# Optimization experiments

Measured on AMD Instinct MI355X. Metric: run time of the kernel, lower is better.

## Reference

```python
import jax, jax.numpy as jnp
import numpy as np

B, S, H = 32, 255, 1024
BS, WD, O = 120, 20, 10
HSZ = 2 * (BS + 1) + WD  # 262


def setup_inputs() -> dict:
    key = jax.random.key(0)
    ks = jax.random.split(key, 9)
    inv = lambda *d: 1.0 / np.sqrt(d[0])
    return {
        "state": jax.random.normal(ks[0], (B, S, H), jnp.float32),
        "head_w": jax.random.normal(ks[1], (H, BS), jnp.float32) * inv(H),
        "head_b": jax.random.normal(ks[2], (BS,), jnp.float32) * 0.02,
        "tail_w": jax.random.normal(ks[3], (H, BS), jnp.float32) * inv(H),
        "tail_b": jax.random.normal(ks[4], (BS,), jnp.float32) * 0.02,
        "U": jax.random.normal(ks[5], (O, BS, BS), jnp.float32) * inv(BS),
        "width_table": jax.random.normal(ks[6], (256, WD), jnp.float32).at[0].set(0.0),  # padding_idx=0
        "cls_w": jax.random.normal(ks[7], (O, HSZ), jnp.float32) * inv(HSZ),
        "cls_b": jax.random.normal(ks[8], (O,), jnp.float32) * 0.02,
    }


def _leaky_relu(x):
    return jnp.where(x >= 0, x, 0.01 * x)  # torch LeakyReLU default slope


def reference(state, head_w, head_b, tail_w, tail_b, U, width_table, cls_w, cls_b):
    b, s, _ = state.shape
    bs = head_w.shape[1]
    # head/tail MLPs (dropout is identity in eval)
    h = _leaky_relu(state @ head_w + head_b)  # (b, s, bs)
    t = _leaky_relu(state @ tail_w + tail_b)  # (b, s, bs)

    # bilinear term
    scores1 = jnp.einsum('bxi,oij,byj->bxyo', h, U, t)  # (b, s, s, O)

    # append bias-ones feature
    ones = jnp.ones((b, s, 1), h.dtype)
    h1 = jnp.concatenate([h, ones], axis=-1)  # (b, s, bs+1)
    t1 = jnp.concatenate([t, ones], axis=-1)

    # span-width embedding: pos[x, y] = y - x + 1, clamped to 0 for y < x
    pos = jnp.arange(s)[None, :] - jnp.arange(s)[:, None] + 1
    pos = pos * (pos > 0)
    wemb = width_table[pos]  # (s, s, WD)

    # cls(concat(h1_x, t1_y, wemb_xy)) decomposed into three small projections
    # + broadcast-add; mathematically identical to materializing affined_cat.
    Wh = cls_w[:, :bs + 1]              # (O, bs+1)
    Wt = cls_w[:, bs + 1:2 * (bs + 1)]  # (O, bs+1)
    Ww = cls_w[:, 2 * (bs + 1):]        # (O, WD)
    scores2 = (jnp.einsum('bxi,oi->bxo', h1, Wh)[:, :, None, :]
               + jnp.einsum('byi,oi->byo', t1, Wt)[:, None, :, :]
               + jnp.einsum('xyw,ow->xyo', wemb, Ww)[None]
               + cls_b)
    return scores1 + scores2
```

## Files before the change

### kernel.cpp

```cpp
#include <hip/hip_runtime.h>
#include <hip/hip_bf16.h>

using f32x4 = __attribute__((ext_vector_type(4))) float;
using s16x8 = __attribute__((ext_vector_type(8))) short;
using s16x4 = __attribute__((ext_vector_type(4))) short;

constexpr int RTOT = 32 * 255;

__device__ inline unsigned short f2bf(float x) {
    __hip_bfloat16 b = __float2bfloat16(x);
    return __builtin_bit_cast(unsigned short, b);
}
__device__ inline float bf2f(unsigned short u) {
    unsigned int t = ((unsigned int)u) << 16;
    return __builtin_bit_cast(float, t);
}
__device__ inline f32x4 mfma16(s16x8 a, s16x8 b, f32x4 c) {
    return __builtin_amdgcn_mfma_f32_16x16x32_bf16(a, b, c, 0, 0, 0);
}
__device__ inline void gload16(const unsigned short* g, unsigned short* l) {
    __builtin_amdgcn_global_load_lds(
        (const __attribute__((address_space(1))) void*)g,
        (__attribute__((address_space(3))) void*)l, 16, 0, 0);
}


__global__ __launch_bounds__(256) void convert_k(
    const float* __restrict__ head_w, const float* __restrict__ tail_w,
    const float* __restrict__ U, const float* __restrict__ wtab,
    const float* __restrict__ cls_w,
    unsigned short* __restrict__ WP, unsigned short* __restrict__ Ut,
    float* __restrict__ tblp)
{
    const int tid = threadIdx.x;
    if (blockIdx.x < 16) {
        __shared__ unsigned short Lw[64][258];
        const int ks = blockIdx.x;
        for (int idx = tid; idx < 64 * 16; idx += 256) {
            int r = idx >> 4, c = idx & 15;
            Lw[r][120 + ((c >= 8) ? 128 : 0) + (c & 7)] = 0;
        }
        for (int idx = tid; idx < 7680; idx += 256) {
            int r = idx / 120, c = idx - r * 120;
            Lw[r][c] = f2bf(head_w[(ks * 64 + r) * 120 + c]);
        }
        for (int idx = tid; idx < 7680; idx += 256) {
            int r = idx / 120, c = idx - r * 120;
            Lw[r][128 + c] = f2bf(tail_w[(ks * 64 + r) * 120 + c]);
        }
        __syncthreads();
        for (int item = tid; item < 2048; item += 256) {
            int n = item >> 3, kcp = item & 7;
            int kc = kcp ^ (n & 7);
            s16x8 v;
            #pragma unroll
            for (int e = 0; e < 8; ++e) v[e] = (short)Lw[kc * 8 + e][n];
            *(s16x8*)&WP[ks * 16384 + item * 8] = v;
        }
    } else {
        int gid = (blockIdx.x - 16) * 256 + tid;
        if (gid < 163840) {
            int j = gid & 127, i2 = (gid >> 7) & 127, o = gid >> 14;
            float v = (i2 < 120 && j < 120) ? U[((size_t)o * 120 + i2) * 120 + j] : 0.f;
            Ut[(size_t)o * 16384 + (size_t)j * 128 + i2] = f2bf(v);
        } else {
            int id = gid - 163840;
            if (id < 2560) {
                int p = id / 10, o = id - (id / 10) * 10;
                float s = 0.f;
                #pragma unroll
                for (int wq = 0; wq < 20; ++wq)
                    s += wtab[p * 20 + wq] * cls_w[o * 262 + 242 + wq];
                tblp[p * 12 + o] = s;
            }
        }
    }
}

__global__ __launch_bounds__(512) void ht_mfma(
    const float* __restrict__ state, const unsigned short* __restrict__ WP,
    const float* __restrict__ head_b, const float* __restrict__ tail_b,
    const float* __restrict__ cls_w, const float* __restrict__ cls_b,
    unsigned short* __restrict__ hbuf, unsigned short* __restrict__ tbuf,
    float* __restrict__ hwp, float* __restrict__ twp)
{
    __shared__ unsigned short Ss[2][32 * 64];
    __shared__ unsigned short Ws[2][256 * 64];
    const int r0 = blockIdx.x * 32;
    const int tid = threadIdx.x;
    const int w = tid >> 6, lane = tid & 63;
    const int l16 = lane & 15, kq = lane >> 4;
    const int srow = (tid >> 3) & 31, skc = tid & 7;
    const bool do_s = tid < 256;
    const float* sp = &state[(size_t)(r0 + srow) * 1024 + skc * 8];

    f32x4 acc[2][2];
    #pragma unroll
    for (int fn = 0; fn < 2; ++fn)
        #pragma unroll
        for (int fr = 0; fr < 2; ++fr) acc[fn][fr] = (f32x4){0.f, 0.f, 0.f, 0.f};

    #pragma unroll
    for (int j = 0; j < 4; ++j) {
        int off = (w * 4 + j) * 512;
        gload16(WP + off + lane * 8, &Ws[0][off]);
    }
    if (do_s) {
        f32x4 a0 = *(const f32x4*)sp;
        f32x4 a1 = *(const f32x4*)(sp + 4);
        s16x8 pk;
        #pragma unroll
        for (int e = 0; e < 4; ++e) { pk[e] = (short)f2bf(a0[e]); pk[e + 4] = (short)f2bf(a1[e]); }
        *(s16x8*)((char*)&Ss[0][0] + srow * 128 + ((skc * 16) ^ ((srow & 7) << 4))) = pk;
    }
    __syncthreads();

    for (int it = 0; it < 16; ++it) {
        const int cur = it & 1;
        f32x4 a0, a1;
        if (it < 15) {
            #pragma unroll
            for (int j = 0; j < 4; ++j) {
                int off = (w * 4 + j) * 512;
                gload16(WP + (it + 1) * 16384 + off + lane * 8, &Ws[cur ^ 1][off]);
            }
            if (do_s) {
                a0 = *(const f32x4*)(sp + (it + 1) * 64);
                a1 = *(const f32x4*)(sp + (it + 1) * 64 + 4);
            }
        }
        const char* SsB = (const char*)&Ss[cur][0];
        const char* WsB = (const char*)&Ws[cur][0];
        s16x8 bf[2][2];
        #pragma unroll
        for (int fr = 0; fr < 2; ++fr) {
            int rr = fr * 16 + l16;
            #pragma unroll
            for (int ks = 0; ks < 2; ++ks)
                bf[fr][ks] = *(const s16x8*)(SsB + rr * 128 + ((ks * 64 + kq * 16) ^ ((rr & 7) << 4)));
        }
        #pragma unroll
        for (int fn = 0; fn < 2; ++fn) {
            int n = w * 32 + fn * 16 + l16;
            #pragma unroll
            for (int ks = 0; ks < 2; ++ks) {
                s16x8 af = *(const s16x8*)(WsB + n * 128 + ((ks * 64 + kq * 16) ^ ((n & 7) << 4)));
                #pragma unroll
                for (int fr = 0; fr < 2; ++fr)
                    acc[fn][fr] = mfma16(af, bf[fr][ks], acc[fn][fr]);
            }
        }
        if (it < 15 && do_s) {
            s16x8 pk;
            #pragma unroll
            for (int e = 0; e < 4; ++e) { pk[e] = (short)f2bf(a0[e]); pk[e + 4] = (short)f2bf(a1[e]); }
            *(s16x8*)((char*)&Ss[cur ^ 1][0] + srow * 128 + ((skc * 16) ^ ((srow & 7) << 4))) = pk;
        }
        __syncthreads();
    }

    unsigned short* Hl = &Ws[0][0];
    unsigned short* Tl = &Ws[1][0];
    #pragma unroll
    for (int fn = 0; fn < 2; ++fn) {
        const int n0 = w * 32 + fn * 16 + kq * 4;
        const int isT = n0 >= 128;
        const int c0 = n0 & 127;
        const int g = c0 >> 3, sub = c0 & 7;
        const float* bp = isT ? tail_b : head_b;
        unsigned short* dstl = isT ? Tl : Hl;
        unsigned short* dstg = isT ? tbuf : hbuf;
        #pragma unroll
        for (int fr = 0; fr < 2; ++fr) {
            const int rloc = fr * 16 + l16;
            const int r = r0 + rloc;
            s16x4 pk;
            #pragma unroll
            for (int e = 0; e < 4; ++e) {
                float bv = (c0 + e < 120) ? bp[c0 + e] : 0.f;
                float z = acc[fn][fr][e] + bv;
                z = (z >= 0.f) ? z : 0.01f * z;
                pk[e] = (short)f2bf(z);
            }
            *(s16x4*)&dstl[rloc * 128 + ((g ^ (rloc & 7)) << 3) + sub] = pk;
            {
                int bq = r / 255, x = r - bq * 255;
                *(s16x4*)&dstg[((size_t)bq * 256 + x) * 128 + ((g ^ (x & 7)) << 3) + sub] = pk;
            }
        }
    }
    __syncthreads();

    float* Wl = (float*)&Ws[0][4096];
    for (int idx = tid; idx < 2430; idx += 512) {
        if (idx < 2420) {
            int which = idx / 1210, rem = idx - which * 1210;
            int o = rem / 121, i = rem - o * 121;
            Wl[idx] = cls_w[o * 262 + which * 121 + i];
        } else Wl[idx] = cls_b[idx - 2420];
    }
    __syncthreads();

    for (int d = tid; d < 640; d += 512) {
        int which = d / 320, rem = d - which * 320;
        int rr = rem / 10, o = rem - rr * 10;
        const unsigned short* row = (which ? Tl : Hl) + rr * 128;
        const float* wp2 = &Wl[which * 1210 + o * 121];
        float s = 0.f;
        #pragma unroll
        for (int c = 0; c < 15; ++c) {
            s16x8 v = *(const s16x8*)&row[(c ^ (rr & 7)) << 3];
            #pragma unroll
            for (int e = 0; e < 8; ++e)
                s += bf2f((unsigned short)v[e]) * wp2[c * 8 + e];
        }
        s += wp2[120];
        int gr = r0 + rr;
        if (!which) hwp[(size_t)gr * 12 + o] = s + Wl[2420 + o];
        else        twp[(size_t)gr * 12 + o] = s;
    }
}

__global__ __launch_bounds__(512) void main_mfma(
    const unsigned short* __restrict__ hbuf, const unsigned short* __restrict__ tbuf,
    const unsigned short* __restrict__ Ut,
    const float* __restrict__ hwp, const float* __restrict__ twp,
    const float* __restrict__ tblp, float* __restrict__ out)
{
    __shared__ __align__(16) char smem[124416];
    unsigned short* hUs = (unsigned short*)smem;
    unsigned short* Bs  = (unsigned short*)smem;
    unsigned short* Hs  = (unsigned short*)(smem + 65536);
    float* Ts = (float*)(smem + 98304);
    float* Tb = (float*)(smem + 110592);
    float* Hw = (float*)(smem + 122880);

    const int wgid = blockIdx.x + (blockIdx.y << 3);
    const int virt = (wgid & 7) * 32 + (wgid >> 3);
    const int b = virt >> 3, mg = virt & 7;
    const int tid = threadIdx.x;
    const int w = tid >> 6, lane = tid & 63;
    const int l16 = lane & 15, kq = lane >> 4;
    const int wm = w >> 2, wy = w & 3;
    const size_t tbase = (size_t)b * 256 * 128;
    const size_t hbase = ((size_t)b * 256 + mg * 32) * 128;

    #pragma unroll
    for (int j = 0; j < 8; ++j) {
        int off = (w * 8 + j) * 512;
        gload16(&tbuf[tbase + off + lane * 8], &Bs[off]);
    }
    gload16(&hbuf[hbase + (size_t)(w * 64 + lane) * 8], &Hs[w * 512]);
    {
        const float* twb = twp + (size_t)b * 3060;
        for (int idx = tid; idx < 3060; idx += 512) Ts[idx] = twb[idx];
        for (int idx = tid; idx < 3072; idx += 512) Tb[idx] = tblp[idx];
        if (tid < 384) {
            int mgl = mg * 384 + tid;
            Hw[tid] = (mgl < 3060) ? hwp[(size_t)b * 3060 + mgl] : 0.f;
        }
    }
    __syncthreads();

    s16x8 bfr[4][4];
    #pragma unroll
    for (int ks = 0; ks < 4; ++ks)
        #pragma unroll
        for (int fy = 0; fy < 4; ++fy) {
            int row = wy * 64 + fy * 16 + l16;
            bfr[ks][fy] = *(const s16x8*)((const char*)Bs + row * 256 +
                           ((ks * 64 + kq * 16) ^ ((row & 7) << 4)));
        }
    s16x8 bh[2][4];
    #pragma unroll
    for (int xf = 0; xf < 2; ++xf) {
        int rr = xf * 16 + l16;
        #pragma unroll
        for (int ks = 0; ks < 4; ++ks)
            bh[xf][ks] = *(const s16x8*)((const char*)Hs + rr * 256 +
                          ((ks * 64 + kq * 16) ^ ((rr & 7) << 4)));
    }
    __syncthreads();

    {
        const int jrow = w * 16 + l16;
        const int j0 = w * 16 + kq * 4;
        const int g2 = j0 >> 3, sub2b = (j0 & 7) * 2;
        #pragma unroll 2
        for (int o = 0; o < 10; ++o) {
            f32x4 acc1[2];
            acc1[0] = (f32x4){0.f, 0.f, 0.f, 0.f};
            acc1[1] = (f32x4){0.f, 0.f, 0.f, 0.f};
            #pragma unroll
            for (int ks = 0; ks < 4; ++ks) {
                s16x8 af = *(const s16x8*)&Ut[(size_t)o * 16384 +
                            (size_t)jrow * 128 + ks * 32 + kq * 8];
                acc1[0] = mfma16(af, bh[0][ks], acc1[0]);
                acc1[1] = mfma16(af, bh[1][ks], acc1[1]);
            }
            #pragma unroll
            for (int xf = 0; xf < 2; ++xf) {
                int mloc = (xf * 16 + l16) * 12 + o;
                s16x4 pk;
                #pragma unroll
                for (int e = 0; e < 4; ++e) pk[e] = (short)f2bf(acc1[xf][e]);
                *(s16x4*)((char*)hUs + mloc * 256 +
                          ((g2 ^ (mloc & 7)) << 4) + sub2b) = pk;
            }
        }
    }
    __syncthreads();

    for (int i = 0; i < 3; ++i) {
        const int mt = i * 128;
        f32x4 acc[4][4];
        #pragma unroll
        for (int fm = 0; fm < 4; ++fm)
            #pragma unroll
            for (int fy = 0; fy < 4; ++fy) acc[fm][fy] = (f32x4){0.f, 0.f, 0.f, 0.f};

        __builtin_amdgcn_s_setprio(1);
        #pragma unroll
        for (int ks = 0; ks < 4; ++ks) {
            s16x8 af[4];
            #pragma unroll
            for (int fm = 0; fm < 4; ++fm) {
                int row = mt + wm * 64 + fm * 16 + l16;
                af[fm] = *(const s16x8*)((const char*)hUs + row * 256 +
                          ((ks * 64 + kq * 16) ^ ((row & 7) << 4)));
            }
            #pragma unroll
            for (int fm = 0; fm < 4; ++fm)
                #pragma unroll
                for (int fy = 0; fy < 4; ++fy)
                    acc[fm][fy] = mfma16(af[fm], bfr[ks][fy], acc[fm][fy]);
        }
        __builtin_amdgcn_s_setprio(0);

        #pragma unroll
        for (int fm = 0; fm < 4; ++fm) {
            const int mloc = mt + wm * 64 + fm * 16 + kq * 4;
            const int xloc = mloc / 12, o0 = mloc % 12;
            const int x = mg * 32 + xloc;
            if (x < 255) {
                const int rx = b * 255 + x;
                f32x4 hv = *(const f32x4*)&Hw[xloc * 12 + o0];
                #pragma unroll
                for (int fy = 0; fy < 4; ++fy) {
                    const int y = wy * 64 + fy * 16 + l16;
                    if (y < 255) {
                        f32x4 tv = *(const f32x4*)&Ts[y * 12 + o0];
                        int p = y - x + 1; if (p < 0) p = 0;
                        f32x4 wv = *(const f32x4*)&Tb[p * 12 + o0];
                        float* op = &out[((size_t)rx * 255 + y) * 10 + o0];
                        if (o0 < 8) {
                            float v[4];
                            #pragma unroll
                            for (int e = 0; e < 4; ++e)
                                v[e] = acc[fm][fy][e] + hv[e] + tv[e] + wv[e];
                            __builtin_memcpy(op, v, 16);
                        } else {
                            float v[2];
                            v[0] = acc[fm][fy][0] + hv[0] + tv[0] + wv[0];
                            v[1] = acc[fm][fy][1] + hv[1] + tv[1] + wv[1];
                            __builtin_memcpy(op, v, 8);
                        }
                    }
                }
            }
        }
    }
}

extern "C" void kernel_launch(void* const* d_in, const int* in_sizes, int n_in,
                              void* d_out, int out_size, void* d_ws, size_t ws_size,
                              hipStream_t stream)
{
    (void)in_sizes; (void)n_in; (void)out_size; (void)ws_size;
    const float* state  = (const float*)d_in[0];
    const float* head_w = (const float*)d_in[1];
    const float* head_b = (const float*)d_in[2];
    const float* tail_w = (const float*)d_in[3];
    const float* tail_b = (const float*)d_in[4];
    const float* U      = (const float*)d_in[5];
    const float* wtab   = (const float*)d_in[6];
    const float* cls_w  = (const float*)d_in[7];
    const float* cls_b  = (const float*)d_in[8];
    float* out = (float*)d_out;

    unsigned short* u16 = (unsigned short*)d_ws;
    unsigned short* tbuf = u16;
    unsigned short* hbuf = tbuf + 1048576;
    unsigned short* WP   = hbuf + 1048576;
    unsigned short* Ut   = WP + 262144;
    float* hwp  = (float*)(Ut + 163840);
    float* twp  = hwp + 97920;
    float* tblp = twp + 97920;

    hipLaunchKernelGGL(convert_k, dim3(666), dim3(256), 0, stream,
                       head_w, tail_w, U, wtab, cls_w, WP, Ut, tblp);
    hipLaunchKernelGGL(ht_mfma, dim3(255), dim3(512), 0, stream,
                       state, WP, head_b, tail_b, cls_w, cls_b,
                       hbuf, tbuf, hwp, twp);
    hipLaunchKernelGGL(main_mfma, dim3(8, 32), dim3(512), 0, stream,
                       hbuf, tbuf, Ut, hwp, twp, tblp, out);
}
```

Baseline: 76.16 us.

## Fuse three kernels into one cooperative persistent kernel with grid syncs

Merges the weight-conversion, head/tail projection and bilinear main kernels into a single cooperative kernel launched with 256 blocks. Grid-wide syncs separate the phases. The aim is to remove launch overhead and inter-kernel gaps. In exchange, all phases share one 124 KB shared-memory allocation and 512-thread launch bounds, which caps occupancy at one block per CU. The conversion phase now runs on only 256 blocks instead of 666, and grid.sync adds its own barrier cost.

```diff
diff --git a/kernel.cpp b/kernel.cpp
--- a/kernel.cpp
+++ b/kernel.cpp
@@ -1,11 +1,12 @@
 #include <hip/hip_runtime.h>
 #include <hip/hip_bf16.h>
+#include <hip/hip_cooperative_groups.h>
+
+namespace cg = cooperative_groups;
 
 using f32x4 = __attribute__((ext_vector_type(4))) float;
 using s16x8 = __attribute__((ext_vector_type(8))) short;
 using s16x4 = __attribute__((ext_vector_type(4))) short;
-
-constexpr int RTOT = 32 * 255;
 
 __device__ inline unsigned short f2bf(float x) {
     __hip_bfloat16 b = __float2bfloat16(x);
@@ -25,31 +26,41 @@
 }
 
 
-__global__ __launch_bounds__(256) void convert_k(
+__global__ __launch_bounds__(512) void mega_k(
+    const float* __restrict__ state,
     const float* __restrict__ head_w, const float* __restrict__ tail_w,
     const float* __restrict__ U, const float* __restrict__ wtab,
-    const float* __restrict__ cls_w,
+    const float* __restrict__ cls_w, const float* __restrict__ cls_b,
+    const float* __restrict__ head_b, const float* __restrict__ tail_b,
     unsigned short* __restrict__ WP, unsigned short* __restrict__ Ut,
-    float* __restrict__ tblp)
+    unsigned short* __restrict__ hbuf, unsigned short* __restrict__ tbuf,
+    float* __restrict__ hwp, float* __restrict__ twp,
+    float* __restrict__ tblp, float* __restrict__ out)
 {
+    cg::grid_group grid = cg::this_grid();
+    __shared__ __align__(16) char smem[124416];
     const int tid = threadIdx.x;
-    if (blockIdx.x < 16) {
-        __shared__ unsigned short Lw[64][258];
-        const int ks = blockIdx.x;
-        for (int idx = tid; idx < 64 * 16; idx += 256) {
+    const int blk = blockIdx.x;
+    const int w = tid >> 6, lane = tid & 63;
+    const int l16 = lane & 15, kq = lane >> 4;
+
+    if (blk < 16) {
+        unsigned short (*Lw)[258] = (unsigned short (*)[258])smem;
+        const int ks = blk;
+        for (int idx = tid; idx < 64 * 16; idx += 512) {
             int r = idx >> 4, c = idx & 15;
             Lw[r][120 + ((c >= 8) ? 128 : 0) + (c & 7)] = 0;
         }
-        for (int idx = tid; idx < 7680; idx += 256) {
+        for (int idx = tid; idx < 7680; idx += 512) {
             int r = idx / 120, c = idx - r * 120;
             Lw[r][c] = f2bf(head_w[(ks * 64 + r) * 120 + c]);
         }
-        for (int idx = tid; idx < 7680; idx += 256) {
+        for (int idx = tid; idx < 7680; idx += 512) {
             int r = idx / 120, c = idx - r * 120;
             Lw[r][128 + c] = f2bf(tail_w[(ks * 64 + r) * 120 + c]);
         }
         __syncthreads();
-        for (int item = tid; item < 2048; item += 256) {
+        for (int item = tid; item < 2048; item += 512) {
             int n = item >> 3, kcp = item & 7;
             int kc = kcp ^ (n & 7);
             s16x8 v;
@@ -58,14 +69,13 @@
             *(s16x8*)&WP[ks * 16384 + item * 8] = v;
         }
     } else {
-        int gid = (blockIdx.x - 16) * 256 + tid;
-        if (gid < 163840) {
-            int j = gid & 127, i2 = (gid >> 7) & 127, o = gid >> 14;
-            float v = (i2 < 120 && j < 120) ? U[((size_t)o * 120 + i2) * 120 + j] : 0.f;
-            Ut[(size_t)o * 16384 + (size_t)j * 128 + i2] = f2bf(v);
-        } else {
-            int id = gid - 163840;
-            if (id < 2560) {
+        for (int idx = (blk - 16) * 512 + tid; idx < 166400; idx += 240 * 512) {
+            if (idx < 163840) {
+                int j = idx & 127, i2 = (idx >> 7) & 127, o = idx >> 14;
+                float v = (i2 < 120 && j < 120) ? U[((size_t)o * 120 + i2) * 120 + j] : 0.f;
+                Ut[(size_t)o * 16384 + (size_t)j * 128 + i2] = f2bf(v);
+            } else {
+                int id = idx - 163840;
                 int p = id / 10, o = id - (id / 10) * 10;
                 float s = 0.f;
                 #pragma unroll
@@ -75,295 +85,284 @@
             }
         }
     }
-}
-
-__global__ __launch_bounds__(512) void ht_mfma(
-    const float* __restrict__ state, const unsigned short* __restrict__ WP,
-    const float* __restrict__ head_b, const float* __restrict__ tail_b,
-    const float* __restrict__ cls_w, const float* __restrict__ cls_b,
-    unsigned short* __restrict__ hbuf, unsigned short* __restrict__ tbuf,
-    float* __restrict__ hwp, float* __restrict__ twp)
-{
-    __shared__ unsigned short Ss[2][32 * 64];
-    __shared__ unsigned short Ws[2][256 * 64];
-    const int r0 = blockIdx.x * 32;
-    const int tid = threadIdx.x;
-    const int w = tid >> 6, lane = tid & 63;
-    const int l16 = lane & 15, kq = lane >> 4;
-    const int srow = (tid >> 3) & 31, skc = tid & 7;
-    const bool do_s = tid < 256;
-    const float* sp = &state[(size_t)(r0 + srow) * 1024 + skc * 8];
-
-    f32x4 acc[2][2];
-    #pragma unroll
-    for (int fn = 0; fn < 2; ++fn)
-        #pragma unroll
-        for (int fr = 0; fr < 2; ++fr) acc[fn][fr] = (f32x4){0.f, 0.f, 0.f, 0.f};
-
-    #pragma unroll
-    for (int j = 0; j < 4; ++j) {
-        int off = (w * 4 + j) * 512;
-        gload16(WP + off + lane * 8, &Ws[0][off]);
+    __threadfence();
+    grid.sync();
+
+    if (blk < 255) {
+        unsigned short* Ss0 = (unsigned short*)smem;
+        unsigned short* Ss1 = (unsigned short*)(smem + 4096);
+        unsigned short* Ws0 = (unsigned short*)(smem + 8192);
+        unsigned short* Ws1 = (unsigned short*)(smem + 8192 + 32768);
+        unsigned short* SsA[2] = {Ss0, Ss1};
+        unsigned short* WsA[2] = {Ws0, Ws1};
+        const int r0 = blk * 32;
+        const int srow = (tid >> 3) & 31, skc = tid & 7;
+        const bool do_s = tid < 256;
+        const float* sp = &state[(size_t)(r0 + srow) * 1024 + skc * 8];
+
+        f32x4 acc[2][2];
+        #pragma unroll
+        for (int fn = 0; fn < 2; ++fn)
+            #pragma unroll
+            for (int fr = 0; fr < 2; ++fr) acc[fn][fr] = (f32x4){0.f, 0.f, 0.f, 0.f};
+
+        #pragma unroll
+        for (int j = 0; j < 4; ++j) {
+            int off = (w * 4 + j) * 512;
+            gload16(WP + off + lane * 8, &Ws0[off]);
+        }
+        if (do_s) {
+            f32x4 a0 = *(const f32x4*)sp;
+            f32x4 a1 = *(const f32x4*)(sp + 4);
+            s16x8 pk;
+            #pragma unroll
+            for (int e = 0; e < 4; ++e) { pk[e] = (short)f2bf(a0[e]); pk[e + 4] = (short)f2bf(a1[e]); }
+            *(s16x8*)((char*)Ss0 + srow * 128 + ((skc * 16) ^ ((srow & 7) << 4))) = pk;
+        }
+        __syncthreads();
+
+        for (int it = 0; it < 16; ++it) {
+            const int cur = it & 1;
+            f32x4 a0, a1;
+            if (it < 15) {
+                #pragma unroll
+                for (int j = 0; j < 4; ++j) {
+                    int off = (w * 4 + j) * 512;
+                    gload16(WP + (it + 1) * 16384 + off + lane * 8, &WsA[cur ^ 1][off]);
+                }
+                if (do_s) {
+                    a0 = *(const f32x4*)(sp + (it + 1) * 64);
+                    a1 = *(const f32x4*)(sp + (it + 1) * 64 + 4);
+                }
+            }
+            const char* SsB = (const char*)SsA[cur];
+            const char* WsB = (const char*)WsA[cur];
+            s16x8 bf[2][2];
+            #pragma unroll
+            for (int fr = 0; fr < 2; ++fr) {
+                int rr = fr * 16 + l16;
+                #pragma unroll
+                for (int ks = 0; ks < 2; ++ks)
+                    bf[fr][ks] = *(const s16x8*)(SsB + rr * 128 + ((ks * 64 + kq * 16) ^ ((rr & 7) << 4)));
+            }
+            #pragma unroll
+            for (int fn = 0; fn < 2; ++fn) {
+                int n = w * 32 + fn * 16 + l16;
+                #pragma unroll
+                for (int ks = 0; ks < 2; ++ks) {
+                    s16x8 af = *(const s16x8*)(WsB + n * 128 + ((ks * 64 + kq * 16) ^ ((n & 7) << 4)));
+                    #pragma unroll
+                    for (int fr = 0; fr < 2; ++fr)
+                        acc[fn][fr] = mfma16(af, bf[fr][ks], acc[fn][fr]);
+                }
+            }
+            if (it < 15 && do_s) {
+                s16x8 pk;
+                #pragma unroll
+                for (int e = 0; e < 4; ++e) { pk[e] = (short)f2bf(a0[e]); pk[e + 4] = (short)f2bf(a1[e]); }
+                *(s16x8*)((char*)SsA[cur ^ 1] + srow * 128 + ((skc * 16) ^ ((srow & 7) << 4))) = pk;
+            }
+            __syncthreads();
+        }
+
+        unsigned short* Hl = Ws0;
+        unsigned short* Tl = Ws1;
+        #pragma unroll
+        for (int fn = 0; fn < 2; ++fn) {
+            const int n0 = w * 32 + fn * 16 + kq * 4;
+            const int isT = n0 >= 128;
+            const int c0 = n0 & 127;
+            const int g = c0 >> 3, sub = c0 & 7;
+            const float* bp = isT ? tail_b : head_b;
+            unsigned short* dstl = isT ? Tl : Hl;
+            unsigned short* dstg = isT ? tbuf : hbuf;
+            #pragma unroll
+            for (int fr = 0; fr < 2; ++fr) {
+                const int rloc = fr * 16 + l16;
+                const int r = r0 + rloc;
+                s16x4 pk;
+                #pragma unroll
+                for (int e = 0; e < 4; ++e) {
+                    float bv = (c0 + e < 120) ? bp[c0 + e] : 0.f;
+                    float z = acc[fn][fr][e] + bv;
+                    z = (z >= 0.f) ? z : 0.01f * z;
+                    pk[e] = (short)f2bf(z);
+                }
+                *(s16x4*)&dstl[rloc * 128 + ((g ^ (rloc & 7)) << 3) + sub] = pk;
+                {
+                    int bq = r / 255, x = r - bq * 255;
+                    *(s16x4*)&dstg[((size_t)bq * 256 + x) * 128 + ((g ^ (x & 7)) << 3) + sub] = pk;
+                }
+            }
+        }
+        __syncthreads();
+
+        float* Wl = (float*)(Ws0 + 4096);
+        for (int idx = tid; idx < 2430; idx += 512) {
+            if (idx < 2420) {
+                int which = idx / 1210, rem = idx - which * 1210;
+                int o = rem / 121, i = rem - o * 121;
+                Wl[idx] = cls_w[o * 262 + which * 121 + i];
+            } else Wl[idx] = cls_b[idx - 2420];
+        }
+        __syncthreads();
+
+        for (int d = tid; d < 640; d += 512) {
+            int which = d / 320, rem = d - which * 320;
+            int rr = rem / 10, o = rem - rr * 10;
+            const unsigned short* row = (which ? Tl : Hl) + rr * 128;
+            const float* wp2 = &Wl[which * 1210 + o * 121];
+            float s = 0.f;
+            #pragma unroll
+            for (int c = 0; c < 15; ++c) {
+                s16x8 v = *(const s16x8*)&row[(c ^ (rr & 7)) << 3];
+                #pragma unroll
+                for (int e = 0; e < 8; ++e)
+                    s += bf2f((unsigned short)v[e]) * wp2[c * 8 + e];
+            }
+            s += wp2[120];
+            int gr = r0 + rr;
+            if (!which) hwp[(size_t)gr * 12 + o] = s + Wl[2420 + o];
+            else        twp[(size_t)gr * 12 + o] = s;
+        }
     }
-    if (do_s) {
-        f32x4 a0 = *(const f32x4*)sp;
-        f32x4 a1 = *(const f32x4*)(sp + 4);
-        s16x8 pk;
-        #pragma unroll
-        for (int e = 0; e < 4; ++e) { pk[e] = (short)f2bf(a0[e]); pk[e + 4] = (short)f2bf(a1[e]); }
-        *(s16x8*)((char*)&Ss[0][0] + srow * 128 + ((skc * 16) ^ ((srow & 7) << 4))) = pk;
-    }
-    __syncthreads();
-
-    for (int it = 0; it < 16; ++it) {
-        const int cur = it & 1;
-        f32x4 a0, a1;
-        if (it < 15) {
-            #pragma unroll
-            for (int j = 0; j < 4; ++j) {
-                int off = (w * 4 + j) * 512;
-                gload16(WP + (it + 1) * 16384 + off + lane * 8, &Ws[cur ^ 1][off]);
-            }
-            if (do_s) {
-                a0 = *(const f32x4*)(sp + (it + 1) * 64);
-                a1 = *(const f32x4*)(sp + (it + 1) * 64 + 4);
-            }
-        }
-        const char* SsB = (const char*)&Ss[cur][0];
-        const char* WsB = (const char*)&Ws[cur][0];
-        s16x8 bf[2][2];
-        #pragma unroll
-        for (int fr = 0; fr < 2; ++fr) {
-            int rr = fr * 16 + l16;
-            #pragma unroll
-            for (int ks = 0; ks < 2; ++ks)
-                bf[fr][ks] = *(const s16x8*)(SsB + rr * 128 + ((ks * 64 + kq * 16) ^ ((rr & 7) << 4)));
-        }
-        #pragma unroll
-        for (int fn = 0; fn < 2; ++fn) {
-            int n = w * 32 + fn * 16 + l16;
-            #pragma unroll
-            for (int ks = 0; ks < 2; ++ks) {
-                s16x8 af = *(const s16x8*)(WsB + n * 128 + ((ks * 64 + kq * 16) ^ ((n & 7) << 4)));
-                #pragma unroll
-                for (int fr = 0; fr < 2; ++fr)
-                    acc[fn][fr] = mfma16(af, bf[fr][ks], acc[fn][fr]);
-            }
-        }
-        if (it < 15 && do_s) {
-            s16x8 pk;
-            #pragma unroll
-            for (int e = 0; e < 4; ++e) { pk[e] = (short)f2bf(a0[e]); pk[e + 4] = (short)f2bf(a1[e]); }
-            *(s16x8*)((char*)&Ss[cur ^ 1][0] + srow * 128 + ((skc * 16) ^ ((srow & 7) << 4))) = pk;
-        }
-        __syncthreads();
-    }
-
-    unsigned short* Hl = &Ws[0][0];
-    unsigned short* Tl = &Ws[1][0];
-    #pragma unroll
-    for (int fn = 0; fn < 2; ++fn) {
-        const int n0 = w * 32 + fn * 16 + kq * 4;
-        const int isT = n0 >= 128;
-        const int c0 = n0 & 127;
-        const int g = c0 >> 3, sub = c0 & 7;
-        const float* bp = isT ? tail_b : head_b;
-        unsigned short* dstl = isT ? Tl : Hl;
-        unsigned short* dstg = isT ? tbuf : hbuf;
-        #pragma unroll
-        for (int fr = 0; fr < 2; ++fr) {
-            const int rloc = fr * 16 + l16;
-            const int r = r0 + rloc;
-            s16x4 pk;
-            #pragma unroll
-            for (int e = 0; e < 4; ++e) {
-                float bv = (c0 + e < 120) ? bp[c0 + e] : 0.f;
-                float z = acc[fn][fr][e] + bv;
-                z = (z >= 0.f) ? z : 0.01f * z;
-                pk[e] = (short)f2bf(z);
-            }
-            *(s16x4*)&dstl[rloc * 128 + ((g ^ (rloc & 7)) << 3) + sub] = pk;
-            {
-                int bq = r / 255, x = r - bq * 255;
-                *(s16x4*)&dstg[((size_t)bq * 256 + x) * 128 + ((g ^ (x & 7)) << 3) + sub] = pk;
-            }
-        }
-    }
-    __syncthreads();
-
-    float* Wl = (float*)&Ws[0][4096];
-    for (int idx = tid; idx < 2430; idx += 512) {
-        if (idx < 2420) {
-            int which = idx / 1210, rem = idx - which * 1210;
-            int o = rem / 121, i = rem - o * 121;
-            Wl[idx] = cls_w[o * 262 + which * 121 + i];
-        } else Wl[idx] = cls_b[idx - 2420];
-    }
-    __syncthreads();
-
-    for (int d = tid; d < 640; d += 512) {
-        int which = d / 320, rem = d - which * 320;
-        int rr = rem / 10, o = rem - rr * 10;
-        const unsigned short* row = (which ? Tl : Hl) + rr * 128;
-        const float* wp2 = &Wl[which * 1210 + o * 121];
-        float s = 0.f;
-        #pragma unroll
-        for (int c = 0; c < 15; ++c) {
-            s16x8 v = *(const s16x8*)&row[(c ^ (rr & 7)) << 3];
-            #pragma unroll
-            for (int e = 0; e < 8; ++e)
-                s += bf2f((unsigned short)v[e]) * wp2[c * 8 + e];
-        }
-        s += wp2[120];
-        int gr = r0 + rr;
-        if (!which) hwp[(size_t)gr * 12 + o] = s + Wl[2420 + o];
-        else        twp[(size_t)gr * 12 + o] = s;
-    }
-}
-
-__global__ __launch_bounds__(512) void main_mfma(
-    const unsigned short* __restrict__ hbuf, const unsigned short* __restrict__ tbuf,
-    const unsigned short* __restrict__ Ut,
-    const float* __restrict__ hwp, const float* __restrict__ twp,
-    const float* __restrict__ tblp, float* __restrict__ out)
-{
-    __shared__ __align__(16) char smem[124416];
-    unsigned short* hUs = (unsigned short*)smem;
-    unsigned short* Bs  = (unsigned short*)smem;
-    unsigned short* Hs  = (unsigned short*)(smem + 65536);
-    float* Ts = (float*)(smem + 98304);
-    float* Tb = (float*)(smem + 110592);
-    float* Hw = (float*)(smem + 122880);
-
-    const int wgid = blockIdx.x + (blockIdx.y << 3);
-    const int virt = (wgid & 7) * 32 + (wgid >> 3);
-    const int b = virt >> 3, mg = virt & 7;
-    const int tid = threadIdx.x;
-    const int w = tid >> 6, lane = tid & 63;
-    const int l16 = lane & 15, kq = lane >> 4;
-    const int wm = w >> 2, wy = w & 3;
-    const size_t tbase = (size_t)b * 256 * 128;
-    const size_t hbase = ((size_t)b * 256 + mg * 32) * 128;
-
-    #pragma unroll
-    for (int j = 0; j < 8; ++j) {
-        int off = (w * 8 + j) * 512;
-        gload16(&tbuf[tbase + off + lane * 8], &Bs[off]);
-    }
-    gload16(&hbuf[hbase + (size_t)(w * 64 + lane) * 8], &Hs[w * 512]);
+    __threadfence();
+    grid.sync();
+
     {
-        const float* twb = twp + (size_t)b * 3060;
-        for (int idx = tid; idx < 3060; idx += 512) Ts[idx] = twb[idx];
-        for (int idx = tid; idx < 3072; idx += 512) Tb[idx] = tblp[idx];
-        if (tid < 384) {
-            int mgl = mg * 384 + tid;
-            Hw[tid] = (mgl < 3060) ? hwp[(size_t)b * 3060 + mgl] : 0.f;
-        }
-    }
-    __syncthreads();
-
-    s16x8 bfr[4][4];
-    #pragma unroll
-    for (int ks = 0; ks < 4; ++ks)
-        #pragma unroll
-        for (int fy = 0; fy < 4; ++fy) {
-            int row = wy * 64 + fy * 16 + l16;
-            bfr[ks][fy] = *(const s16x8*)((const char*)Bs + row * 256 +
-                           ((ks * 64 + kq * 16) ^ ((row & 7) << 4)));
-        }
-    s16x8 bh[2][4];
-    #pragma unroll
-    for (int xf = 0; xf < 2; ++xf) {
-        int rr = xf * 16 + l16;
+        unsigned short* hUs = (unsigned short*)smem;
+        unsigned short* Bs  = (unsigned short*)smem;
+        unsigned short* Hs  = (unsigned short*)(smem + 65536);
+        float* Ts = (float*)(smem + 98304);
+        float* Tb = (float*)(smem + 110592);
+        float* Hw = (float*)(smem + 122880);
+
+        const int virt = (blk & 7) * 32 + (blk >> 3);
+        const int b = virt >> 3, mg = virt & 7;
+        const int wm = w >> 2, wy = w & 3;
+        const size_t tbase = (size_t)b * 256 * 128;
+        const size_t hbase = ((size_t)b * 256 + mg * 32) * 128;
+
+        #pragma unroll
+        for (int j = 0; j < 8; ++j) {
+            int off = (w * 8 + j) * 512;
+            gload16(&tbuf[tbase + off + lane * 8], &Bs[off]);
+        }
+        gload16(&hbuf[hbase + (size_t)(w * 64 + lane) * 8], &Hs[w * 512]);
+        {
+            const float* twb = twp + (size_t)b * 3060;
+            for (int idx = tid; idx < 3060; idx += 512) Ts[idx] = twb[idx];
+            for (int idx = tid; idx < 3072; idx += 512) Tb[idx] = tblp[idx];
+            if (tid < 384) {
+                int mgl = mg * 384 + tid;
+                Hw[tid] = (mgl < 3060) ? hwp[(size_t)b * 3060 + mgl] : 0.f;
+            }
+        }
+        __syncthreads();
+
+        s16x8 bfr[4][4];
         #pragma unroll
         for (int ks = 0; ks < 4; ++ks)
-            bh[xf][ks] = *(const s16x8*)((const char*)Hs + rr * 256 +
-                          ((ks * 64 + kq * 16) ^ ((rr & 7) << 4)));
-    }
-    __syncthreads();
-
-    {
-        const int jrow = w * 16 + l16;
-        const int j0 = w * 16 + kq * 4;
-        const int g2 = j0 >> 3, sub2b = (j0 & 7) * 2;
-        #pragma unroll 2
-        for (int o = 0; o < 10; ++o) {
-            f32x4 acc1[2];
-            acc1[0] = (f32x4){0.f, 0.f, 0.f, 0.f};
-            acc1[1] = (f32x4){0.f, 0.f, 0.f, 0.f};
+            #pragma unroll
+            for (int fy = 0; fy < 4; ++fy) {
+                int row = wy * 64 + fy * 16 + l16;
+                bfr[ks][fy] = *(const s16x8*)((const char*)Bs + row * 256 +
+                               ((ks * 64 + kq * 16) ^ ((row & 7) << 4)));
+            }
+        s16x8 bh[2][4];
+        #pragma unroll
+        for (int xf = 0; xf < 2; ++xf) {
+            int rr = xf * 16 + l16;
+            #pragma unroll
+            for (int ks = 0; ks < 4; ++ks)
+                bh[xf][ks] = *(const s16x8*)((const char*)Hs + rr * 256 +
+                              ((ks * 64 + kq * 16) ^ ((rr & 7) << 4)));
+        }
+        __syncthreads();
+
+        {
+            const int jrow = w * 16 + l16;
+            const int j0 = w * 16 + kq * 4;
+            const int g2 = j0 >> 3, sub2b = (j0 & 7) * 2;
+            #pragma unroll 2
+            for (int o = 0; o < 10; ++o) {
+                f32x4 acc1[2];
+                acc1[0] = (f32x4){0.f, 0.f, 0.f, 0.f};
+                acc1[1] = (f32x4){0.f, 0.f, 0.f, 0.f};
+                #pragma unroll
+                for (int ks = 0; ks < 4; ++ks) {
+                    s16x8 af = *(const s16x8*)&Ut[(size_t)o * 16384 +
+                                (size_t)jrow * 128 + ks * 32 + kq * 8];
+                    acc1[0] = mfma16(af, bh[0][ks], acc1[0]);
+                    acc1[1] = mfma16(af, bh[1][ks], acc1[1]);
+                }
+                #pragma unroll
+                for (int xf = 0; xf < 2; ++xf) {
+                    int mloc = (xf * 16 + l16) * 12 + o;
+                    s16x4 pk;
+                    #pragma unroll
+                    for (int e = 0; e < 4; ++e) pk[e] = (short)f2bf(acc1[xf][e]);
+                    *(s16x4*)((char*)hUs + mloc * 256 +
+                              ((g2 ^ (mloc & 7)) << 4) + sub2b) = pk;
+                }
+            }
+        }
+        __syncthreads();
+
+        for (int i = 0; i < 3; ++i) {
+            const int mt = i * 128;
+            f32x4 acc[4][4];
+            #pragma unroll
+            for (int fm = 0; fm < 4; ++fm)
+                #pragma unroll
+                for (int fy = 0; fy < 4; ++fy) acc[fm][fy] = (f32x4){0.f, 0.f, 0.f, 0.f};
+
+            __builtin_amdgcn_s_setprio(1);
             #pragma unroll
             for (int ks = 0; ks < 4; ++ks) {
-                s16x8 af = *(const s16x8*)&Ut[(size_t)o * 16384 +
-                            (size_t)jrow * 128 + ks * 32 + kq * 8];
-                acc1[0] = mfma16(af, bh[0][ks], acc1[0]);
-                acc1[1] = mfma16(af, bh[1][ks], acc1[1]);
-            }
-            #pragma unroll
-            for (int xf = 0; xf < 2; ++xf) {
-                int mloc = (xf * 16 + l16) * 12 + o;
-                s16x4 pk;
-                #pragma unroll
-                for (int e = 0; e < 4; ++e) pk[e] = (short)f2bf(acc1[xf][e]);
-                *(s16x4*)((char*)hUs + mloc * 256 +
-                          ((g2 ^ (mloc & 7)) << 4) + sub2b) = pk;
-            }
-        }
-    }
-    __syncthreads();
-
-    for (int i = 0; i < 3; ++i) {
-        const int mt = i * 128;
-        f32x4 acc[4][4];
-        #pragma unroll
-        for (int fm = 0; fm < 4; ++fm)
-            #pragma unroll
-            for (int fy = 0; fy < 4; ++fy) acc[fm][fy] = (f32x4){0.f, 0.f, 0.f, 0.f};
-
-        __builtin_amdgcn_s_setprio(1);
-        #pragma unroll
-        for (int ks = 0; ks < 4; ++ks) {
-            s16x8 af[4];
+                s16x8 af[4];
+                #pragma unroll
+                for (int fm = 0; fm < 4; ++fm) {
+                    int row = mt + wm * 64 + fm * 16 + l16;
+                    af[fm] = *(const s16x8*)((const char*)hUs + row * 256 +
+                              ((ks * 64 + kq * 16) ^ ((row & 7) << 4)));
+                }
+                #pragma unroll
+                for (int fm = 0; fm < 4; ++fm)
+                    #pragma unroll
+                    for (int fy = 0; fy < 4; ++fy)
+                        acc[fm][fy] = mfma16(af[fm], bfr[ks][fy], acc[fm][fy]);
+            }
+            __builtin_amdgcn_s_setprio(0);
+
             #pragma unroll
             for (int fm = 0; fm < 4; ++fm) {
-                int row = mt + wm * 64 + fm * 16 + l16;
-                af[fm] = *(const s16x8*)((const char*)hUs + row * 256 +
-                          ((ks * 64 + kq * 16) ^ ((row & 7) << 4)));
-            }
-            #pragma unroll
-            for (int fm = 0; fm < 4; ++fm)
-                #pragma unroll
-                for (int fy = 0; fy < 4; ++fy)
-                    acc[fm][fy] = mfma16(af[fm], bfr[ks][fy], acc[fm][fy]);
-        }
-        __builtin_amdgcn_s_setprio(0);
-
-        #pragma unroll
-        for (int fm = 0; fm < 4; ++fm) {
-            const int mloc = mt + wm * 64 + fm * 16 + kq * 4;
-            const int xloc = mloc / 12, o0 = mloc % 12;
-            const int x = mg * 32 + xloc;
-            if (x < 255) {
-                const int rx = b * 255 + x;
-                f32x4 hv = *(const f32x4*)&Hw[xloc * 12 + o0];
-                #pragma unroll
-                for (int fy = 0; fy < 4; ++fy) {
-                    const int y = wy * 64 + fy * 16 + l16;
-                    if (y < 255) {
-                        f32x4 tv = *(const f32x4*)&Ts[y * 12 + o0];
-                        int p = y - x + 1; if (p < 0) p = 0;
-                        f32x4 wv = *(const f32x4*)&Tb[p * 12 + o0];
-                        float* op = &out[((size_t)rx * 255 + y) * 10 + o0];
-                        if (o0 < 8) {
-                            float v[4];
-                            #pragma unroll
-                            for (int e = 0; e < 4; ++e)
-                                v[e] = acc[fm][fy][e] + hv[e] + tv[e] + wv[e];
-                            __builtin_memcpy(op, v, 16);
-                        } else {
-                            float v[2];
-                            v[0] = acc[fm][fy][0] + hv[0] + tv[0] + wv[0];
-                            v[1] = acc[fm][fy][1] + hv[1] + tv[1] + wv[1];
-                            __builtin_memcpy(op, v, 8);
+                const int mloc = mt + wm * 64 + fm * 16 + kq * 4;
+                const int xloc = mloc / 12, o0 = mloc % 12;
+                const int x = mg * 32 + xloc;
+                if (x < 255) {
+                    const int rx = b * 255 + x;
+                    f32x4 hv = *(const f32x4*)&Hw[xloc * 12 + o0];
+                    #pragma unroll
+                    for (int fy = 0; fy < 4; ++fy) {
+                        const int y = wy * 64 + fy * 16 + l16;
+                        if (y < 255) {
+                            f32x4 tv = *(const f32x4*)&Ts[y * 12 + o0];
+                            int p = y - x + 1; if (p < 0) p = 0;
+                            f32x4 wv = *(const f32x4*)&Tb[p * 12 + o0];
+                            float* op = &out[((size_t)rx * 255 + y) * 10 + o0];
+                            if (o0 < 8) {
+                                float v[4];
+                                #pragma unroll
+                                for (int e = 0; e < 4; ++e)
+                                    v[e] = acc[fm][fy][e] + hv[e] + tv[e] + wv[e];
+                                __builtin_memcpy(op, v, 16);
+                            } else {
+                                float v[2];
+                                v[0] = acc[fm][fy][0] + hv[0] + tv[0] + wv[0];
+                                v[1] = acc[fm][fy][1] + hv[1] + tv[1] + wv[1];
+                                __builtin_memcpy(op, v, 8);
+                            }
                         }
                     }
                 }
@@ -397,11 +396,13 @@
     float* twp  = hwp + 97920;
     float* tblp = twp + 97920;
 
-    hipLaunchKernelGGL(convert_k, dim3(666), dim3(256), 0, stream,
-                       head_w, tail_w, U, wtab, cls_w, WP, Ut, tblp);
-    hipLaunchKernelGGL(ht_mfma, dim3(255), dim3(512), 0, stream,
-                       state, WP, head_b, tail_b, cls_w, cls_b,
-                       hbuf, tbuf, hwp, twp);
-    hipLaunchKernelGGL(main_mfma, dim3(8, 32), dim3(512), 0, stream,
-                       hbuf, tbuf, Ut, hwp, twp, tblp, out);
-}
+    void* args[] = {
+        (void*)&state, (void*)&head_w, (void*)&tail_w, (void*)&U,
+        (void*)&wtab, (void*)&cls_w, (void*)&cls_b,
+        (void*)&head_b, (void*)&tail_b,
+        (void*)&WP, (void*)&Ut, (void*)&hbuf, (void*)&tbuf,
+        (void*)&hwp, (void*)&twp, (void*)&tblp, (void*)&out
+    };
+    hipLaunchCooperativeKernel((const void*)mega_k, dim3(256), dim3(512),
+                               args, 0, stream);
+}
```

After: 236.3 us. +210.3%, slower.
